# Performance work log

Measured on AMD Instinct MI355X. Metric: run time of the kernel, lower is better.

Reference implementation:

```python
import jax, jax.numpy as jnp
import numpy as np

B, T, N, FIN = 32, 12, 1024, 64
K, OUT_F = 3, 64


def setup_inputs() -> dict:
    key = jax.random.key(0)
    k1, k2, k3 = jax.random.split(key, 3)
    x = jax.random.normal(k1, (B, T, N, FIN), dtype=jnp.float32)
    A = jax.random.uniform(k2, (B, N, N), dtype=jnp.float32)
    # Xavier-uniform-like init for Theta [K, in_f, out_f]
    limit = float(np.sqrt(6.0 / (FIN + OUT_F)))
    Theta = jax.random.uniform(k3, (K, FIN, OUT_F), dtype=jnp.float32,
                               minval=-limit, maxval=limit)
    return {"x": x, "A": A, "Theta": Theta}


def reference(x, A, Theta):
    Bb, Tt, Nn, Fin = x.shape
    Kk = Theta.shape[0]
    I = jnp.broadcast_to(jnp.eye(Nn, dtype=x.dtype), (Bb, Nn, Nn))
    # lambda_max = max row-sum of A, clamped to >= 1
    lambda_max = jnp.maximum(jnp.max(jnp.sum(A, axis=-1), axis=-1), 1.0)
    L = 2.0 * A / lambda_max[:, None, None] - I  # scaled Laplacian surrogate [B,N,N]
    out = jnp.zeros((Bb, Tt, Nn, Theta.shape[-1]), dtype=x.dtype)
    T_prev2, T_prev = None, I
    for k in range(Kk):  # small fixed K-hop loop
        if k == 0:
            T_k = I
        elif k == 1:
            T_k = L
        else:
            T_k = 2.0 * jnp.einsum('bnm,bmp->bnp', L, T_prev) - T_prev2
        T_prev2, T_prev = T_prev, T_k
        rhs = jnp.einsum('btnf,fo->btno', x, Theta[k])   # feature transform
        out = out + jnp.einsum('bnm,btmo->btno', T_k, rhs)  # graph aggregation
    return jax.nn.relu(out)
```

## Files before the change

### kernel.cpp

```cpp
#include <hip/hip_runtime.h>

typedef unsigned short ushort_t;
typedef unsigned char uchar_t;
typedef __attribute__((ext_vector_type(8))) __bf16 bf16x8;
typedef __attribute__((ext_vector_type(4))) float f32x4;
typedef __attribute__((ext_vector_type(8))) unsigned short u16x8;
typedef __attribute__((ext_vector_type(8))) int i32x8;

#define NB 32
#define TT 12
#define NNODE 1024
#define FF 64
#define OO 64
#define TO 768

#define SCL_ONE 127

__device__ __forceinline__ unsigned short f2bf(float f) {
    unsigned u = __float_as_uint(f);
    u += 0x7FFFu + ((u >> 16) & 1u);
    return (unsigned short)(u >> 16);
}
__device__ __forceinline__ float bf2f(unsigned short h) {
    return __uint_as_float(((unsigned)h) << 16);
}
__device__ __forceinline__ unsigned char f2fp8(float f) {
    return (unsigned char)(__builtin_amdgcn_cvt_pk_fp8_f32(f, f, 0, false) & 0xff);
}

__device__ __forceinline__ void gload16(const void* g, void* l) {
    __builtin_amdgcn_global_load_lds(
        (const __attribute__((address_space(1))) unsigned int*)g,
        (__attribute__((address_space(3))) unsigned int*)l, 16, 0, 0);
}

__global__ __launch_bounds__(256) void k_prep(const float* __restrict__ A,
                                              float* __restrict__ rsum,
                                              uchar_t* __restrict__ E8) {
    __shared__ float ls[4];
    const size_t idx = ((size_t)blockIdx.x * 256 + threadIdx.x) * 8;
    const float4 v0 = *(const float4*)(A + idx);
    const float4 v1 = *(const float4*)(A + idx + 4);
    unsigned lo = 0, hi = 0;
    lo = (unsigned)__builtin_amdgcn_cvt_pk_fp8_f32(v0.x * 2.0f, v0.y * 2.0f, (int)lo, false);
    lo = (unsigned)__builtin_amdgcn_cvt_pk_fp8_f32(v0.z * 2.0f, v0.w * 2.0f, (int)lo, true);
    hi = (unsigned)__builtin_amdgcn_cvt_pk_fp8_f32(v1.x * 2.0f, v1.y * 2.0f, (int)hi, false);
    hi = (unsigned)__builtin_amdgcn_cvt_pk_fp8_f32(v1.z * 2.0f, v1.w * 2.0f, (int)hi, true);
    uint2 pk; pk.x = lo; pk.y = hi;
    *(uint2*)(E8 + idx) = pk;
    float s = v0.x + v0.y + v0.z + v0.w + v1.x + v1.y + v1.z + v1.w;
#pragma unroll
    for (int off = 32; off > 0; off >>= 1) s += __shfl_down(s, off, 64);
    const int w = threadIdx.x >> 6;
    if ((threadIdx.x & 63) == 0) ls[w] = s;
    __syncthreads();
    if (threadIdx.x == 0) {
        rsum[blockIdx.x * 2]     = ls[0] + ls[1];
        rsum[blockIdx.x * 2 + 1] = ls[2] + ls[3];
    }
}

__global__ __launch_bounds__(256) void k_lmax(const float* __restrict__ rsum,
                                              unsigned* __restrict__ lam) {
    __shared__ float ls[4];
    const int b = blockIdx.x;
    const float4 v = *(const float4*)(rsum + b * NNODE + threadIdx.x * 4);
    float m = fmaxf(fmaxf(v.x, v.y), fmaxf(v.z, v.w));
#pragma unroll
    for (int off = 32; off > 0; off >>= 1) m = fmaxf(m, __shfl_down(m, off, 64));
    const int w = threadIdx.x >> 6;
    if ((threadIdx.x & 63) == 0) ls[w] = m;
    __syncthreads();
    if (threadIdx.x == 0) {
        const float r = fmaxf(fmaxf(ls[0], ls[1]), fmaxf(ls[2], ls[3]));
        lam[b] = __float_as_uint(fmaxf(r, 1.0f));
    }
}

__global__ void k_theta(const float* __restrict__ Th, ushort_t* __restrict__ Tht) {
    int tid = blockIdx.x * 256 + threadIdx.x;
    if (tid < 3 * 64 * 64) {
        int k = tid >> 12, rem = tid & 4095, o = rem >> 6, f = rem & 63;
        Tht[tid] = f2bf(Th[(k << 12) + (f << 6) + o]);
    }
}

__global__ __launch_bounds__(512, 5) void k_feature(const float* __restrict__ x,
                                                    const ushort_t* __restrict__ Tht,
                                                    ushort_t* __restrict__ Pb,
                                                    ushort_t* __restrict__ Qc,
                                                    uchar_t* __restrict__ R2f8) {
    __shared__ __align__(16) uchar_t th[3 * 64 * 128];
    __shared__ __align__(16) uchar_t tbuf[26624];
    ushort_t* tbq = (ushort_t*)tbuf;
    char* tbr = (char*)(tbuf + 17408);

    const int n0 = blockIdx.x * 128;
    const int t = blockIdx.y;
    const int b = blockIdx.z;
    const int tid = threadIdx.x;
    const int w = tid >> 6, lane = tid & 63, quad = lane >> 4, l15 = lane & 15;

#pragma unroll
    for (int i = 0; i < 3; ++i) {
        int chunk = i * 512 + tid;
        int ko = chunk >> 3, c = chunk & 7;
        int phys = c ^ (ko & 7);
        const int4 v = *(const int4*)(Tht + ko * 64 + c * 8);
        *(int4*)(th + ko * 128 + phys * 16) = v;
    }

    const float* xr = x + (((size_t)b * TT + t) * NNODE + n0 + w * 16 + l15) * FF;
    bf16x8 af[2];
#pragma unroll
    for (int ks = 0; ks < 2; ++ks) {
        const float4 v0 = *(const float4*)(xr + ks * 32 + quad * 8);
        const float4 v1 = *(const float4*)(xr + ks * 32 + quad * 8 + 4);
        u16x8 p;
        p[0] = f2bf(v0.x); p[1] = f2bf(v0.y); p[2] = f2bf(v0.z); p[3] = f2bf(v0.w);
        p[4] = f2bf(v1.x); p[5] = f2bf(v1.y); p[6] = f2bf(v1.z); p[7] = f2bf(v1.w);
        af[ks] = *(bf16x8*)&p;
    }
    __syncthreads();

    f32x4 acc[3][4];
#pragma unroll
    for (int k = 0; k < 3; ++k)
#pragma unroll
        for (int cb = 0; cb < 4; ++cb) acc[k][cb] = (f32x4){0.f, 0.f, 0.f, 0.f};

#pragma unroll
    for (int k = 0; k < 3; ++k)
#pragma unroll
        for (int ks = 0; ks < 2; ++ks)
#pragma unroll
            for (int cb = 0; cb < 4; ++cb) {
                const int o = cb * 16 + l15;
                const int c = (ks * 4 + quad) ^ (o & 7);
                const bf16x8 bfr = *(const bf16x8*)(th + (k * 64 + o) * 128 + c * 16);
                acc[k][cb] = __builtin_amdgcn_mfma_f32_16x16x32_bf16(af[ks], bfr, acc[k][cb], 0, 0, 0);
            }

    ushort_t* Pbb = Pb + (((size_t)b * TT + t) * NNODE + n0) * OO;
#pragma unroll
    for (int cb = 0; cb < 4; ++cb)
#pragma unroll
        for (int r = 0; r < 4; ++r) {
            const int n = w * 16 + quad * 4 + r;
            const int o = cb * 16 + l15;
            Pbb[(size_t)n * OO + o] = f2bf(acc[0][cb][r] - acc[2][cb][r]);
        }

#pragma unroll
    for (int cb = 0; cb < 4; ++cb)
#pragma unroll
        for (int r = 0; r < 4; ++r) {
            const int nl = w * 16 + quad * 4 + r;
            const int o = cb * 16 + l15;
            tbq[o * 136 + nl] = f2bf(acc[1][cb][r] - 2.0f * acc[2][cb][r]);
            tbr[o * 144 + nl] = (char)f2fp8(acc[2][cb][r]);
        }
    __syncthreads();

    {
        const int o = tid >> 3, seg = tid & 7;
        ushort_t* qrow = Qc + ((size_t)b * TO + t * 64 + o) * NNODE + n0 + seg * 16;
        const ushort_t* sq = tbq + o * 136 + seg * 16;
        *(u16x8*)(qrow) = *(const u16x8*)(sq);
        *(u16x8*)(qrow + 8) = *(const u16x8*)(sq + 8);
        uchar_t* rrow = R2f8 + ((size_t)b * TO + t * 64 + o) * NNODE + n0 + seg * 16;
        *(int4*)rrow = *(const int4*)(tbr + o * 144 + seg * 16);
    }
}

template <int MODE>
__global__ __launch_bounds__(256, 3) void k_gemm8(const uchar_t* __restrict__ Aop, size_t aBS,
                                                  const uchar_t* __restrict__ Bop, size_t bBS,
                                                  const unsigned* __restrict__ lam,
                                                  const ushort_t* __restrict__ Qc,
                                                  uchar_t* __restrict__ Zf8,
                                                  ushort_t* __restrict__ Pbp,
                                                  float* __restrict__ outp) {
    __shared__ __align__(16) uchar_t smem[49152];
    const int bid = blockIdx.x;
    const int xcd = bid & 7, y = bid >> 3;
    const int tile = y % 48;
    const int b = xcd + 8 * (y / 48);
    const int tm = (MODE == 1) ? (tile >> 3) : (tile / 6);
    const int tn = (MODE == 1) ? (tile & 7) : (tile % 6);
    const int m0 = tm * 128, n0 = tn * 128;
    const int tid = threadIdx.x;
    const int w = tid >> 6, lane = tid & 63, quad = lane >> 4, l15 = lane & 15;
    const int wr = w >> 1, wc = w & 1;
    const uchar_t* Ab = Aop + (size_t)b * aBS + (size_t)m0 * NNODE;
    const uchar_t* Bb = Bop + (size_t)b * bBS + (size_t)n0 * NNODE;
    const float lamf = __uint_as_float(lam[b]);

    int ldso[4];
    size_t goff[4];
#pragma unroll
    for (int i = 0; i < 4; ++i) {
        int slot = i * 256 + tid;
        int row = slot >> 3;
        int lc = (slot & 7) ^ (row & 7);
        ldso[i] = slot * 16;
        goff[i] = (size_t)row * NNODE + lc * 16;
    }

    f32x4 acc[4][4];
#pragma unroll
    for (int i = 0; i < 4; ++i)
#pragma unroll
        for (int j = 0; j < 4; ++j) acc[i][j] = (f32x4){0.f, 0.f, 0.f, 0.f};

#pragma unroll
    for (int i = 0; i < 4; ++i) gload16(Ab + goff[i], smem + ldso[i]);
#pragma unroll
    for (int i = 0; i < 4; ++i) gload16(Bb + goff[i], smem + 16384 + ldso[i]);

#pragma unroll
    for (int kk = 0; kk < 8; ++kk) {
        const uchar_t* At = smem;
        const uchar_t* Bt = smem + 16384 + ((kk & 1) << 14);
        uchar_t* Btn = smem + 16384 + (((kk & 1) ^ 1) << 14);
        if (kk < 7) {
            const int k0 = (kk + 1) << 7;
#pragma unroll
            for (int i = 0; i < 4; ++i) gload16(Bb + k0 + goff[i], Btn + ldso[i]);
            asm volatile("s_waitcnt vmcnt(4)" ::: "memory");
        } else {
            asm volatile("s_waitcnt vmcnt(0)" ::: "memory");
        }
        __builtin_amdgcn_s_barrier();

        i32x8 af[4], bfr[4];
#pragma unroll
        for (int i = 0; i < 4; ++i) {
            const int m = wr * 64 + i * 16 + l15;
            const int n = wc * 64 + i * 16 + l15;
            const int4 alo = *(const int4*)(At + m * 128 + (((quad << 1)) ^ (m & 7)) * 16);
            const int4 ahi = *(const int4*)(At + m * 128 + (((quad << 1) | 1) ^ (m & 7)) * 16);
            const int4 blo = *(const int4*)(Bt + n * 128 + (((quad << 1)) ^ (n & 7)) * 16);
            const int4 bhi = *(const int4*)(Bt + n * 128 + (((quad << 1) | 1) ^ (n & 7)) * 16);
            af[i] = (i32x8){alo.x, alo.y, alo.z, alo.w, ahi.x, ahi.y, ahi.z, ahi.w};
            bfr[i] = (i32x8){blo.x, blo.y, blo.z, blo.w, bhi.x, bhi.y, bhi.z, bhi.w};
        }
        asm volatile("s_waitcnt lgkmcnt(0)" ::: "memory");
        __builtin_amdgcn_s_barrier();
        if (kk < 7) {
            const int k0 = (kk + 1) << 7;
#pragma unroll
            for (int i = 0; i < 4; ++i) gload16(Ab + k0 + goff[i], smem + ldso[i]);
        }
        __builtin_amdgcn_s_setprio(1);
#pragma unroll
        for (int i = 0; i < 4; ++i)
#pragma unroll
            for (int j = 0; j < 4; ++j)
                acc[i][j] = __builtin_amdgcn_mfma_scale_f32_16x16x128_f8f6f4(
                    af[i], bfr[j], acc[i][j], 0, 0, 0, SCL_ONE, 0, SCL_ONE);
        __builtin_amdgcn_s_setprio(0);
    }
    __syncthreads();

    if (MODE == 1) {
        const float c1 = 2.0f / lamf;
        ushort_t* tb = (ushort_t*)smem;
        const ushort_t* Qb = Qc + (size_t)b * TO * NNODE;
        uchar_t* Zb = Zf8 + (size_t)b * TO * NNODE;
#pragma unroll
        for (int i = 0; i < 4; ++i)
#pragma unroll
            for (int r = 0; r < 4; ++r) {
                const int cl = wr * 64 + i * 16 + quad * 4 + r;
                const int c = m0 + cl;
#pragma unroll
                for (int j = 0; j < 4; ++j) {
                    const int nl = wc * 64 + j * 16 + l15;
                    const size_t zi = (size_t)c * NNODE + n0 + nl;
                    const float z = bf2f(Qb[zi]) + c1 * acc[i][j][r];
                    Zb[zi] = f2fp8(z);
                    tb[nl * 136 + cl] = f2bf(z);
                }
            }
        __syncthreads();
        const int t0 = m0 >> 6;
        const int row = tid >> 1, half = tid & 1;
        ushort_t* prow = Pbp + (((size_t)b * TT + t0 + half) * NNODE + n0 + row) * OO;
        const ushort_t* srow = tb + row * 136 + half * 64;
#pragma unroll
        for (int s = 0; s < 8; ++s) {
            u16x8 pv = *(const u16x8*)(prow + s * 8);
            u16x8 zv = *(const u16x8*)(srow + s * 8);
            u16x8 rv;
#pragma unroll
            for (int e = 0; e < 8; ++e) rv[e] = f2bf(bf2f(pv[e]) - bf2f(zv[e]));
            *(u16x8*)(prow + s * 8) = rv;
        }
    } else {
        const float c2 = 1.0f / lamf;
#pragma unroll
        for (int i = 0; i < 4; ++i)
#pragma unroll
            for (int r = 0; r < 4; ++r) {
                const int n = m0 + wr * 64 + i * 16 + quad * 4 + r;
#pragma unroll
                for (int j = 0; j < 4; ++j) {
                    const int c = n0 + wc * 64 + j * 16 + l15;
                    const int t = c >> 6, o = c & 63;
                    const size_t id = (((size_t)b * TT + t) * NNODE + n) * OO + o;
                    outp[id] = fmaxf(bf2f(Pbp[id]) + c2 * acc[i][j][r], 0.0f);
                }
            }
    }
}

extern "C" void kernel_launch(void* const* d_in, const int* in_sizes, int n_in,
                              void* d_out, int out_size, void* d_ws, size_t ws_size,
                              hipStream_t stream) {
    const float* x = (const float*)d_in[0];
    const float* A = (const float*)d_in[1];
    const float* Th = (const float*)d_in[2];
    float* out = (float*)d_out;
    char* ws = (char*)d_ws;

    unsigned* lam = (unsigned*)ws;
    uchar_t* E8 = (uchar_t*)(ws + 256);
    uchar_t* R2f8 = E8 + (size_t)NB * NNODE * NNODE;
    uchar_t* Zf8 = R2f8 + (size_t)NB * TO * NNODE;
    ushort_t* Qc = (ushort_t*)(Zf8 + (size_t)NB * TO * NNODE);
    ushort_t* Pb = Qc + (size_t)NB * TO * NNODE;
    ushort_t* Tht = Pb + (size_t)NB * TT * NNODE * OO;
    float* rsum = (float*)(Tht + 3 * 64 * 64);

    k_prep<<<16384, 256, 0, stream>>>(A, rsum, E8);
    k_lmax<<<NB, 256, 0, stream>>>(rsum, lam);
    k_theta<<<48, 256, 0, stream>>>(Th, Tht);
    k_feature<<<dim3(8, 12, 32), 512, 0, stream>>>(x, Tht, Pb, Qc, R2f8);
    k_gemm8<1><<<1536, 256, 0, stream>>>(R2f8, (size_t)TO * NNODE,
                                         E8, (size_t)NNODE * NNODE,
                                         lam, Qc, Zf8, Pb, nullptr);
    k_gemm8<2><<<1536, 256, 0, stream>>>(E8, (size_t)NNODE * NNODE,
                                         Zf8, (size_t)TO * NNODE,
                                         lam, nullptr, nullptr, Pb, out);
}
```

Before: 401.8 us.

## Enlarge FP8 GEMM tiles to 256x128 with 8 waves and double-buffered A

```diff
diff --git a/kernel.cpp b/kernel.cpp
--- a/kernel.cpp
+++ b/kernel.cpp
@@ -174,21 +174,21 @@
 }
 
 template <int MODE>
-__global__ __launch_bounds__(256, 3) void k_gemm8(const uchar_t* __restrict__ Aop, size_t aBS,
+__global__ __launch_bounds__(512, 2) void k_gemm8(const uchar_t* __restrict__ Aop, size_t aBS,
                                                   const uchar_t* __restrict__ Bop, size_t bBS,
                                                   const unsigned* __restrict__ lam,
                                                   const ushort_t* __restrict__ Qc,
                                                   uchar_t* __restrict__ Zf8,
                                                   ushort_t* __restrict__ Pbp,
                                                   float* __restrict__ outp) {
-    __shared__ __align__(16) uchar_t smem[49152];
+    __shared__ __align__(16) uchar_t smem[98304];
     const int bid = blockIdx.x;
     const int xcd = bid & 7, y = bid >> 3;
-    const int tile = y % 48;
-    const int b = xcd + 8 * (y / 48);
+    const int tile = y % 24;
+    const int b = xcd + 8 * (y / 24);
     const int tm = (MODE == 1) ? (tile >> 3) : (tile / 6);
     const int tn = (MODE == 1) ? (tile & 7) : (tile % 6);
-    const int m0 = tm * 128, n0 = tn * 128;
+    const int m0 = tm * 256, n0 = tn * 128;
     const int tid = threadIdx.x;
     const int w = tid >> 6, lane = tid & 63, quad = lane >> 4, l15 = lane & 15;
     const int wr = w >> 1, wc = w & 1;
@@ -196,15 +196,23 @@
     const uchar_t* Bb = Bop + (size_t)b * bBS + (size_t)n0 * NNODE;
     const float lamf = __uint_as_float(lam[b]);
 
-    int ldso[4];
-    size_t goff[4];
+    int aldo[4], bldo[2];
+    size_t aoff[4], boff[2];
 #pragma unroll
     for (int i = 0; i < 4; ++i) {
-        int slot = i * 256 + tid;
+        int slot = i * 512 + tid;
         int row = slot >> 3;
         int lc = (slot & 7) ^ (row & 7);
-        ldso[i] = slot * 16;
-        goff[i] = (size_t)row * NNODE + lc * 16;
+        aldo[i] = slot * 16;
+        aoff[i] = (size_t)row * NNODE + lc * 16;
+    }
+#pragma unroll
+    for (int i = 0; i < 2; ++i) {
+        int slot = i * 512 + tid;
+        int row = slot >> 3;
+        int lc = (slot & 7) ^ (row & 7);
+        bldo[i] = slot * 16;
+        boff[i] = (size_t)row * NNODE + lc * 16;
     }
 
     f32x4 acc[4][4];
@@ -214,52 +222,70 @@
         for (int j = 0; j < 4; ++j) acc[i][j] = (f32x4){0.f, 0.f, 0.f, 0.f};
 
 #pragma unroll
-    for (int i = 0; i < 4; ++i) gload16(Ab + goff[i], smem + ldso[i]);
-#pragma unroll
-    for (int i = 0; i < 4; ++i) gload16(Bb + goff[i], smem + 16384 + ldso[i]);
+    for (int i = 0; i < 4; ++i) gload16(Ab + aoff[i], smem + aldo[i]);
+#pragma unroll
+    for (int i = 0; i < 2; ++i) gload16(Bb + boff[i], smem + 65536 + bldo[i]);
 
 #pragma unroll
     for (int kk = 0; kk < 8; ++kk) {
-        const uchar_t* At = smem;
-        const uchar_t* Bt = smem + 16384 + ((kk & 1) << 14);
-        uchar_t* Btn = smem + 16384 + (((kk & 1) ^ 1) << 14);
+        const uchar_t* At = smem + ((kk & 1) << 15);
+        const uchar_t* Bt = smem + 65536 + ((kk & 1) << 14);
         if (kk < 7) {
+            uchar_t* An = smem + (((kk + 1) & 1) << 15);
+            uchar_t* Bn = smem + 65536 + (((kk + 1) & 1) << 14);
             const int k0 = (kk + 1) << 7;
 #pragma unroll
-            for (int i = 0; i < 4; ++i) gload16(Bb + k0 + goff[i], Btn + ldso[i]);
-            asm volatile("s_waitcnt vmcnt(4)" ::: "memory");
+            for (int i = 0; i < 4; ++i) gload16(Ab + k0 + aoff[i], An + aldo[i]);
+#pragma unroll
+            for (int i = 0; i < 2; ++i) gload16(Bb + k0 + boff[i], Bn + bldo[i]);
+            asm volatile("s_waitcnt vmcnt(6)" ::: "memory");
         } else {
             asm volatile("s_waitcnt vmcnt(0)" ::: "memory");
         }
         __builtin_amdgcn_s_barrier();
 
         i32x8 af[4], bfr[4];
-#pragma unroll
-        for (int i = 0; i < 4; ++i) {
-            const int m = wr * 64 + i * 16 + l15;
-            const int n = wc * 64 + i * 16 + l15;
-            const int4 alo = *(const int4*)(At + m * 128 + (((quad << 1)) ^ (m & 7)) * 16);
-            const int4 ahi = *(const int4*)(At + m * 128 + (((quad << 1) | 1) ^ (m & 7)) * 16);
-            const int4 blo = *(const int4*)(Bt + n * 128 + (((quad << 1)) ^ (n & 7)) * 16);
-            const int4 bhi = *(const int4*)(Bt + n * 128 + (((quad << 1) | 1) ^ (n & 7)) * 16);
-            af[i] = (i32x8){alo.x, alo.y, alo.z, alo.w, ahi.x, ahi.y, ahi.z, ahi.w};
-            bfr[i] = (i32x8){blo.x, blo.y, blo.z, blo.w, bhi.x, bhi.y, bhi.z, bhi.w};
-        }
+#define LDA(i) { const int m = wr * 64 + (i) * 16 + l15;                                   \
+                 const int4 lo = *(const int4*)(At + m * 128 + (((quad << 1)) ^ (m & 7)) * 16);      \
+                 const int4 hi = *(const int4*)(At + m * 128 + (((quad << 1) | 1) ^ (m & 7)) * 16);  \
+                 af[i] = (i32x8){lo.x, lo.y, lo.z, lo.w, hi.x, hi.y, hi.z, hi.w}; }
+#define LDB(j) { const int n = wc * 64 + (j) * 16 + l15;                                   \
+                 const int4 lo = *(const int4*)(Bt + n * 128 + (((quad << 1)) ^ (n & 7)) * 16);      \
+                 const int4 hi = *(const int4*)(Bt + n * 128 + (((quad << 1) | 1) ^ (n & 7)) * 16);  \
+                 bfr[j] = (i32x8){lo.x, lo.y, lo.z, lo.w, hi.x, hi.y, hi.z, hi.w}; }
+#define MM(i, j) acc[i][j] = __builtin_amdgcn_mfma_scale_f32_16x16x128_f8f6f4( \
+                     af[i], bfr[j], acc[i][j], 0, 0, 0, SCL_ONE, 0, SCL_ONE);
+
+        LDA(0) LDA(1) LDB(0) LDB(1)
+        __builtin_amdgcn_s_barrier();
         asm volatile("s_waitcnt lgkmcnt(0)" ::: "memory");
-        __builtin_amdgcn_s_barrier();
-        if (kk < 7) {
-            const int k0 = (kk + 1) << 7;
-#pragma unroll
-            for (int i = 0; i < 4; ++i) gload16(Ab + k0 + goff[i], smem + ldso[i]);
-        }
+        __builtin_amdgcn_sched_barrier(0);
         __builtin_amdgcn_s_setprio(1);
-#pragma unroll
-        for (int i = 0; i < 4; ++i)
-#pragma unroll
-            for (int j = 0; j < 4; ++j)
-                acc[i][j] = __builtin_amdgcn_mfma_scale_f32_16x16x128_f8f6f4(
-                    af[i], bfr[j], acc[i][j], 0, 0, 0, SCL_ONE, 0, SCL_ONE);
+        MM(0, 0) MM(0, 1) MM(1, 0) MM(1, 1)
         __builtin_amdgcn_s_setprio(0);
+        __builtin_amdgcn_s_barrier();
+        LDA(2) LDA(3)
+        __builtin_amdgcn_s_barrier();
+        asm volatile("s_waitcnt lgkmcnt(0)" ::: "memory");
+        __builtin_amdgcn_sched_barrier(0);
+        __builtin_amdgcn_s_setprio(1);
+        MM(2, 0) MM(2, 1) MM(3, 0) MM(3, 1)
+        __builtin_amdgcn_s_setprio(0);
+        __builtin_amdgcn_s_barrier();
+        LDB(2) LDB(3)
+        __builtin_amdgcn_s_barrier();
+        asm volatile("s_waitcnt lgkmcnt(0)" ::: "memory");
+        __builtin_amdgcn_sched_barrier(0);
+        __builtin_amdgcn_s_setprio(1);
+        MM(0, 2) MM(0, 3) MM(1, 2) MM(1, 3)
+        __builtin_amdgcn_s_setprio(0);
+        __builtin_amdgcn_s_barrier();
+        __builtin_amdgcn_s_setprio(1);
+        MM(2, 2) MM(2, 3) MM(3, 2) MM(3, 3)
+        __builtin_amdgcn_s_setprio(0);
+#undef LDA
+#undef LDB
+#undef MM
     }
     __syncthreads();
 
@@ -280,14 +306,14 @@
                     const size_t zi = (size_t)c * NNODE + n0 + nl;
                     const float z = bf2f(Qb[zi]) + c1 * acc[i][j][r];
                     Zb[zi] = f2fp8(z);
-                    tb[nl * 136 + cl] = f2bf(z);
+                    tb[nl * 264 + cl] = f2bf(z);
                 }
             }
         __syncthreads();
         const int t0 = m0 >> 6;
-        const int row = tid >> 1, half = tid & 1;
-        ushort_t* prow = Pbp + (((size_t)b * TT + t0 + half) * NNODE + n0 + row) * OO;
-        const ushort_t* srow = tb + row * 136 + half * 64;
+        const int row = tid >> 2, tq = tid & 3;
+        ushort_t* prow = Pbp + (((size_t)b * TT + t0 + tq) * NNODE + n0 + row) * OO;
+        const ushort_t* srow = tb + row * 264 + tq * 64;
 #pragma unroll
         for (int s = 0; s < 8; ++s) {
             u16x8 pv = *(const u16x8*)(prow + s * 8);
@@ -337,10 +363,10 @@
     k_lmax<<<NB, 256, 0, stream>>>(rsum, lam);
     k_theta<<<48, 256, 0, stream>>>(Th, Tht);
     k_feature<<<dim3(8, 12, 32), 512, 0, stream>>>(x, Tht, Pb, Qc, R2f8);
-    k_gemm8<1><<<1536, 256, 0, stream>>>(R2f8, (size_t)TO * NNODE,
-                                         E8, (size_t)NNODE * NNODE,
-                                         lam, Qc, Zf8, Pb, nullptr);
-    k_gemm8<2><<<1536, 256, 0, stream>>>(E8, (size_t)NNODE * NNODE,
-                                         Zf8, (size_t)TO * NNODE,
-                                         lam, nullptr, nullptr, Pb, out);
-}
+    k_gemm8<1><<<768, 512, 0, stream>>>(R2f8, (size_t)TO * NNODE,
+                                        E8, (size_t)NNODE * NNODE,
+                                        lam, Qc, Zf8, Pb, nullptr);
+    k_gemm8<2><<<768, 512, 0, stream>>>(E8, (size_t)NNODE * NNODE,
+                                        Zf8, (size_t)TO * NNODE,
+                                        lam, nullptr, nullptr, Pb, out);
+}
```

New measurement: 427.2 us. +6.3%, slower.
